# Optimization experiments

Hardware: AMD Instinct MI355X
Metric: run time of the kernel (lower is better)

Reference implementation:

```python
import jax, jax.numpy as jnp
import numpy as np

# config (from UnifiedAttentionConfig defaults)
D = 512; H = 8; C = 64; DQ = 256; NI = 2; CI = 64
TOPK = 32; LMAX = 16; NWIN = 128; ROPE_BASE = 10000.0
B = 1; T = 1024; LP = 8; P = T // LP
NEG = -1e30


def _rope_cache(seq_len, dim):
    half = dim // 2
    inv = 1.0 / (ROPE_BASE ** (jnp.arange(half, dtype=jnp.float32) / half))
    f = jnp.arange(seq_len, dtype=jnp.float32)[:, None] * inv[None, :]
    emb = jnp.concatenate([f, f], axis=-1)
    return jnp.cos(emb), jnp.sin(emb)


def _rot(x, cos, sin):
    half = x.shape[-1] // 2
    x1, x2 = x[..., :half], x[..., half:]
    return x * cos + jnp.concatenate([-x2, x1], axis=-1) * sin


def _rms(x, w, eps=1e-6):
    return x * jax.lax.rsqrt(jnp.mean(x * x, axis=-1, keepdims=True) + eps) * w


def _forward(h, W_dq, W_uq, W_csa_kv, W_csa_z, B_csa, W_idx_kv, W_idx_z, B_idx,
             W_iuq, W_w, W_swkv, qnorm_w, knorm_w, W_o, sink_logits,
             phrase_mask, phrase_token_idx, phrase_end_pos):
    Bq, Tq, Dq = h.shape
    Pn, Lmax = phrase_mask.shape[1], phrase_mask.shape[2]
    scale = 1.0 / jnp.sqrt(jnp.float32(C))
    cos, sin = _rope_cache(Tq, C)
    cos_i, sin_i = _rope_cache(Tq, CI)
    # ---- queries: compress -> up-project -> RMSNorm -> RoPE (per-token) ----
    q_lat = h @ W_dq                                      # (B,T,DQ)
    q = (q_lat @ W_uq).reshape(Bq, Tq, H, C)
    q = _rot(_rms(q, qnorm_w), cos[:, None, :], sin[:, None, :])
    # ---- gather phrase tokens ----
    idx = phrase_token_idx.reshape(Bq, Pn * Lmax)
    hp = jnp.take_along_axis(h, idx[:, :, None], axis=1).reshape(Bq, Pn, Lmax, Dq)
    m = phrase_mask                                       # (B,P,Lmax) bool
    # ---- multi-head phrase compression (CSA KV) ----
    c_tok = (hp @ W_csa_kv).reshape(Bq, Pn, Lmax, H, C)
    z = (hp @ W_csa_z).reshape(Bq, Pn, Lmax, H, C) + B_csa[None, None]
    z = jnp.where(m[..., None, None], z, NEG)
    g = jax.nn.softmax(z, axis=2)
    g = jnp.where(m.any(axis=2)[:, :, None, None, None], g, 0.0)
    c_csa = jnp.sum(g * c_tok, axis=2)                    # (B,P,H,C) values
    pos = jnp.clip(phrase_end_pos, 0, Tq - 1)
    k_csa = _rot(_rms(c_csa, knorm_w), cos[pos][:, :, None, :], sin[pos][:, :, None, :])
    # ---- single-head phrase compression (indexer keys) ----
    ck = hp @ W_idx_kv                                    # (B,P,Lmax,CI)
    zk = hp @ W_idx_z + B_idx[None, None]
    zk = jnp.where(m[..., None], zk, NEG)
    gk = jax.nn.softmax(zk, axis=2)
    gk = jnp.where(m.any(axis=2)[:, :, None, None], gk, 0.0)
    k_idx = jnp.sum(gk * ck, axis=2)                      # (B,P,CI)
    k_idx = _rot(k_idx, cos_i[pos], sin_i[pos])
    # ---- lightning indexer + causal top-k routing ----
    q_i = (q_lat @ W_iuq).reshape(Bq, Tq, NI, CI)
    s = jax.nn.relu(jnp.einsum('bthd,bpd->bthp', q_i, k_idx))
    I = jnp.sum(s * (h @ W_w)[..., None], axis=2)         # (B,T,P)
    t_idx = jnp.arange(Tq)
    valid = (phrase_end_pos[:, None, :] <= t_idx[None, :, None]) & (phrase_end_pos[:, None, :] >= 0)
    I = jnp.where(valid, I, NEG)
    vals, sel = jax.lax.top_k(I, TOPK)                    # (B,T,K)
    sel_ok = vals > NEG * 0.5
    k_sel = jnp.take_along_axis(k_csa[:, None], sel[:, :, :, None, None], axis=2)  # (B,T,K,H,C)
    v_sel = jnp.take_along_axis(c_csa[:, None], sel[:, :, :, None, None], axis=2)
    logit_csa = jnp.einsum('bthc,btkhc->bthk', q, k_sel) * scale
    logit_csa = jnp.where(sel_ok[:, :, None, :], logit_csa, NEG)
    # ---- sliding window (fixed mode) ----
    kv = (h @ W_swkv).reshape(Bq, Tq, H, C)
    k_sw = _rot(_rms(kv, knorm_w), cos[:, None, :], sin[:, None, :])
    widx = t_idx[:, None] + jnp.arange(NWIN)[None, :] - (NWIN - 1)  # (T,W)
    w_ok = widx >= 0
    widx_c = jnp.clip(widx, 0, Tq - 1)
    k_win = k_sw[:, widx_c]                               # (B,T,W,H,C)
    v_win = kv[:, widx_c]
    logit_sw = jnp.einsum('bthc,btwhc->bthw', q, k_win) * scale
    logit_sw = jnp.where(w_ok[None, :, None, :], logit_sw, NEG)
    # ---- single softmax over [csa | window | sink] ----
    sink = jnp.broadcast_to(sink_logits.reshape(1, 1, H, 1), (Bq, Tq, H, 1))
    pattn = jax.nn.softmax(jnp.concatenate([logit_csa, logit_sw, sink], axis=-1), axis=-1)
    out = jnp.einsum('bthk,btkhc->bthc', pattn[..., :TOPK], v_sel) \
        + jnp.einsum('bthw,btwhc->bthc', pattn[..., TOPK:TOPK + NWIN], v_win)
    return out.reshape(Bq, Tq, H * C) @ W_o


def setup_inputs() -> dict:
    key = jax.random.key(0)
    ks = jax.random.split(key, 16)
    nrm = lambda k, shp: 0.02 * jax.random.normal(k, shp, dtype=jnp.float32)
    # structured phrases: phrase p covers tokens [p*LP, p*LP+LP), padded to LMAX
    l = np.arange(LMAX)
    mask = np.broadcast_to(l < LP, (B, P, LMAX)).copy()
    tok = np.minimum(l, LP - 1)[None, :] + (np.arange(P) * LP)[:, None]
    tok = np.broadcast_to(tok, (B, P, LMAX)).copy()
    end = np.broadcast_to(np.arange(P) * LP + LP - 1, (B, P)).copy()
    pid = np.broadcast_to(np.arange(T) // LP, (B, T)).copy()
    return {
        'h': jax.random.normal(ks[0], (B, T, D), dtype=jnp.float32),
        'phrase_mask': jnp.asarray(mask, dtype=bool),
        'phrase_token_idx': jnp.asarray(tok, dtype=jnp.int32),
        'phrase_end_pos': jnp.asarray(end, dtype=jnp.int32),
        'phrase_id': jnp.asarray(pid, dtype=jnp.int32),
        'W_dq': nrm(ks[1], (D, DQ)),
        'W_uq': nrm(ks[2], (DQ, H * C)),
        'W_csa_kv': nrm(ks[3], (D, H * C)),
        'W_csa_z': nrm(ks[4], (D, H * C)),
        'B_csa': nrm(ks[5], (LMAX, H, C)),
        'W_idx_kv': nrm(ks[6], (D, CI)),
        'W_idx_z': nrm(ks[7], (D, CI)),
        'B_idx': nrm(ks[8], (LMAX, CI)),
        'W_iuq': nrm(ks[9], (DQ, NI * CI)),
        'W_w': nrm(ks[10], (D, NI)),
        'W_swkv': nrm(ks[11], (D, H * C)),
        'qnorm_w': jnp.ones((C,), dtype=jnp.float32),
        'knorm_w': jnp.ones((C,), dtype=jnp.float32),
        'W_o': nrm(ks[12], (H * C, D)),
        'sink_logits': nrm(ks[13], (H,)),
    }


def reference(h, phrase_mask, phrase_token_idx, phrase_end_pos, phrase_id,
              W_dq, W_uq, W_csa_kv, W_csa_z, B_csa, W_idx_kv, W_idx_z, B_idx,
              W_iuq, W_w, W_swkv, qnorm_w, knorm_w, W_o, sink_logits):
    del phrase_id  # only used when sw_mode == 'phrase'
    return _forward(h, W_dq, W_uq, W_csa_kv, W_csa_z, B_csa, W_idx_kv, W_idx_z,
                    B_idx, W_iuq, W_w, W_swkv, qnorm_w, knorm_w, W_o, sink_logits,
                    phrase_mask, phrase_token_idx, phrase_end_pos)
```

## Files before the change

kernel.cpp:

```cpp
#include <hip/hip_runtime.h>
#include <cmath>

static constexpr int Tn = 1024, Dn = 512, Hn = 8, Cn = 64, DQn = 256,
                     NIn = 2, CIn = 64, TK = 32, LM = 16, NW = 128, Pn = 128;
#define NEGV (-1e30f)

typedef unsigned short u16;
typedef __bf16 bf16x8 __attribute__((ext_vector_type(8)));
typedef float f32x4 __attribute__((ext_vector_type(4)));

__device__ __forceinline__ u16 f2bf(float x) {
  unsigned u = __float_as_uint(x);
  return (u16)((u + 0x7fffu + ((u >> 16) & 1u)) >> 16);
}
__device__ __forceinline__ float bf2f(u16 b) {
  return __uint_as_float((unsigned)b << 16);
}

struct PackJobs {
  const float* src[7];
  u16* dst[7];
  int start[8];
  int N[7];
  int logN[7];
  int isA[7];
  int ps[7];
};

__global__ __launch_bounds__(256) void pack_all(PackJobs pj) {
  int i = blockIdx.x * 256 + threadIdx.x;
  if (i >= pj.start[7]) return;
  int j = 0;
  while (i >= pj.start[j + 1]) ++j;
  int local = i - pj.start[j];
  const float* s = pj.src[j];
  u16* dh = pj.dst[j];
  u16* dl = dh + pj.ps[j];
  float x[8];
  size_t idx;
  if (pj.isA[j]) {
    int m = local & 1023;
    int kg = local >> 10;
    const float4* p = reinterpret_cast<const float4*>(s + (size_t)m * 512 + kg * 8);
    float4 a = p[0], b = p[1];
    x[0] = a.x; x[1] = a.y; x[2] = a.z; x[3] = a.w;
    x[4] = b.x; x[5] = b.y; x[6] = b.z; x[7] = b.w;
    idx = ((size_t)kg * 1024 + m) * 8;
  } else {
    int N = pj.N[j];
    int n = local & (N - 1);
    int kg = local >> pj.logN[j];
#pragma unroll
    for (int e = 0; e < 8; ++e) x[e] = s[(size_t)(kg * 8 + e) * N + n];
    idx = ((size_t)kg * N + n) * 8;
  }
  union { u16 u[8]; int4 v; } oh, ol;
#pragma unroll
  for (int e = 0; e < 8; ++e) {
    u16 hb = f2bf(x[e]);
    oh.u[e] = hb;
    ol.u[e] = f2bf(x[e] - bf2f(hb));
  }
  *reinterpret_cast<int4*>(dh + idx) = oh.v;
  *reinterpret_cast<int4*>(dl + idx) = ol.v;
}

struct TileDesc {
  const u16* Blo;
  const u16* Bhi;
  float* Clo;
  float* Chi;
  u16* Cp;
  int ldNlo, ldNhi, ldClo, ldChi, mode, n0, bps, cpps;
};
struct GemmArgs {
  TileDesc d[15];
};

#define GLD16(gp, lp)                                                     \
  __builtin_amdgcn_global_load_lds(                                      \
      (const __attribute__((address_space(1))) unsigned int*)(gp),       \
      (__attribute__((address_space(3))) unsigned int*)(lp), 16, 0, 0)

__global__ __launch_bounds__(256) void gemm_bf16(const u16* __restrict__ Ap,
                                                 int NK, int aps, GemmArgs ga) {
  const int ct = blockIdx.x, rt = blockIdx.y;
  const TileDesc d = ga.d[ct];
  const int m0 = rt * 128;
  __shared__ __align__(16) u16 lA[2][2][4][128][8];
  __shared__ __align__(16) u16 lB[2][2][4][128][8];
  const int tid = threadIdx.x;
  const int w = tid >> 6, lane = tid & 63;
  const int wm = w >> 1, wn = w & 1;

  f32x4 acc[4][4];
#pragma unroll
  for (int a = 0; a < 4; ++a)
#pragma unroll
    for (int b = 0; b < 4; ++b)
#pragma unroll
      for (int r = 0; r < 4; ++r) acc[a][b][r] = 0.f;

  auto stage = [&](int buf, int kg) {
    GLD16(Ap + ((size_t)kg * 1024 + m0 + lane) * 8, &lA[buf][0][w][0][0]);
    GLD16(Ap + ((size_t)kg * 1024 + m0 + 64 + lane) * 8, &lA[buf][0][w][64][0]);
    GLD16(Ap + aps + ((size_t)kg * 1024 + m0 + lane) * 8, &lA[buf][1][w][0][0]);
    GLD16(Ap + aps + ((size_t)kg * 1024 + m0 + 64 + lane) * 8, &lA[buf][1][w][64][0]);
    GLD16(d.Blo + ((size_t)kg * d.ldNlo + lane) * 8, &lB[buf][0][w][0][0]);
    GLD16(d.Bhi + ((size_t)kg * d.ldNhi + lane) * 8, &lB[buf][0][w][64][0]);
    GLD16(d.Blo + d.bps + ((size_t)kg * d.ldNlo + lane) * 8, &lB[buf][1][w][0][0]);
    GLD16(d.Bhi + d.bps + ((size_t)kg * d.ldNhi + lane) * 8, &lB[buf][1][w][64][0]);
  };

  stage(0, w);
  const int kq = lane >> 4, fr = lane & 15;
  for (int ks = 0; ks < NK; ++ks) {
    __syncthreads();
    if (ks + 1 < NK) stage((ks + 1) & 1, (ks + 1) * 4 + w);
    const int cb = ks & 1;
    bf16x8 aFh[4], aFl[4], bFh[4], bFl[4];
#pragma unroll
    for (int f = 0; f < 4; ++f) {
      aFh[f] = *reinterpret_cast<const bf16x8*>(&lA[cb][0][kq][wm * 64 + f * 16 + fr][0]);
      aFl[f] = *reinterpret_cast<const bf16x8*>(&lA[cb][1][kq][wm * 64 + f * 16 + fr][0]);
      bFh[f] = *reinterpret_cast<const bf16x8*>(&lB[cb][0][kq][wn * 64 + f * 16 + fr][0]);
      bFl[f] = *reinterpret_cast<const bf16x8*>(&lB[cb][1][kq][wn * 64 + f * 16 + fr][0]);
    }
#pragma unroll
    for (int fm = 0; fm < 4; ++fm)
#pragma unroll
      for (int fn = 0; fn < 4; ++fn) {
        acc[fm][fn] = __builtin_amdgcn_mfma_f32_16x16x32_bf16(aFh[fm], bFh[fn],
                                                              acc[fm][fn], 0, 0, 0);
        acc[fm][fn] = __builtin_amdgcn_mfma_f32_16x16x32_bf16(aFl[fm], bFh[fn],
                                                              acc[fm][fn], 0, 0, 0);
        acc[fm][fn] = __builtin_amdgcn_mfma_f32_16x16x32_bf16(aFh[fm], bFl[fn],
                                                              acc[fm][fn], 0, 0, 0);
      }
  }
  float* Cb = (wn == 0) ? d.Clo : d.Chi;
  const int ldc = (wn == 0) ? d.ldClo : d.ldChi;
  if (d.mode != 1) {
#pragma unroll
    for (int fm = 0; fm < 4; ++fm)
#pragma unroll
      for (int fn = 0; fn < 4; ++fn)
#pragma unroll
        for (int r = 0; r < 4; ++r) {
          int row = m0 + wm * 64 + fm * 16 + (lane >> 4) * 4 + r;
          int cl = fn * 16 + fr;
          Cb[(size_t)row * ldc + cl] = acc[fm][fn][r];
        }
  }
  if (d.mode >= 1) {
#pragma unroll
    for (int fm = 0; fm < 4; ++fm)
#pragma unroll
      for (int fn = 0; fn < 4; ++fn)
#pragma unroll
        for (int r = 0; r < 4; ++r) {
          int row = m0 + wm * 64 + fm * 16 + (lane >> 4) * 4 + r;
          int gc = d.n0 + wn * 64 + fn * 16 + fr;
          float v = acc[fm][fn][r];
          u16 hb = f2bf(v);
          u16 lb = f2bf(v - bf2f(hb));
          size_t idx = ((size_t)(gc >> 3) * 1024 + row) * 8 + (gc & 7);
          d.Cp[idx] = hb;
          d.Cp[idx + d.cpps] = lb;
        }
  }
}

__global__ __launch_bounds__(256) void idx_kernel(
    const float* __restrict__ h, const float* __restrict__ q_lat,
    const float* __restrict__ Wikv, const float* __restrict__ Wiz,
    const float* __restrict__ Wiuq, float* __restrict__ hikv,
    float* __restrict__ hiz, float* __restrict__ qib) {
  const int t0 = blockIdx.x * 4;
  const int tid = threadIdx.x;
  __shared__ float hs[4][Dn];
  __shared__ float ql[4][DQn];
  for (int i = tid; i < 4 * Dn; i += 256)
    hs[i >> 9][i & 511] = h[(size_t)(t0 + (i >> 9)) * Dn + (i & 511)];
  for (int i = tid; i < 4 * DQn; i += 256)
    ql[i >> 8][i & 255] = q_lat[(size_t)(t0 + (i >> 8)) * DQn + (i & 255)];
  __syncthreads();
  if (tid < 128) {
    const float* Wm = (tid < 64) ? Wikv : Wiz;
    const int ci = tid & 63;
    float a0 = 0.f, a1 = 0.f, a2 = 0.f, a3 = 0.f;
#pragma unroll 8
    for (int k = 0; k < Dn; ++k) {
      float wv = Wm[k * CIn + ci];
      a0 += hs[0][k] * wv;
      a1 += hs[1][k] * wv;
      a2 += hs[2][k] * wv;
      a3 += hs[3][k] * wv;
    }
    float* dst = (tid < 64) ? hikv : hiz;
    dst[(size_t)(t0 + 0) * CIn + ci] = a0;
    dst[(size_t)(t0 + 1) * CIn + ci] = a1;
    dst[(size_t)(t0 + 2) * CIn + ci] = a2;
    dst[(size_t)(t0 + 3) * CIn + ci] = a3;
  } else {
    const int jj = tid - 128;
    float a0 = 0.f, a1 = 0.f, a2 = 0.f, a3 = 0.f;
#pragma unroll 8
    for (int k = 0; k < DQn; ++k) {
      float wv = Wiuq[k * 128 + jj];
      a0 += ql[0][k] * wv;
      a1 += ql[1][k] * wv;
      a2 += ql[2][k] * wv;
      a3 += ql[3][k] * wv;
    }
    qib[(size_t)(t0 + 0) * 128 + jj] = a0;
    qib[(size_t)(t0 + 1) * 128 + jj] = a1;
    qib[(size_t)(t0 + 2) * 128 + jj] = a2;
    qib[(size_t)(t0 + 3) * 128 + jj] = a3;
  }
}

__global__ __launch_bounds__(512) void phrase_rope_kernel(
    const int* __restrict__ maskbuf, const int* __restrict__ tokbuf,
    const int* __restrict__ endbuf, const float* __restrict__ hckv,
    const float* __restrict__ hcz, const float* __restrict__ hikv,
    const float* __restrict__ hiz, const float* __restrict__ Bcsa,
    const float* __restrict__ Bidx, const float* __restrict__ knw,
    const float* __restrict__ qnw, float* __restrict__ ccsa,
    float* __restrict__ kcsa, float* __restrict__ kidx,
    float* __restrict__ q, const float* __restrict__ kv,
    float* __restrict__ ksw) {
  const int tid = threadIdx.x;
  const int c = tid & 63;
  const float sgn = (c < 32) ? -1.f : 1.f;

  if (blockIdx.x >= Pn) {
    const int t = blockIdx.x - Pn;
    const float fr = (float)t * powf(10000.0f, -(float)(c & 31) / 32.0f);
    const float cv = cosf(fr), sv = sinf(fr);
    {
      float x = q[t * Dn + tid];
      float ss = x * x;
#pragma unroll
      for (int off = 32; off; off >>= 1) ss += __shfl_xor(ss, off, 64);
      float xr = x * rsqrtf(ss / (float)Cn + 1e-6f) * qnw[c];
      float pr = __shfl_xor(xr, 32, 64);
      q[t * Dn + tid] = xr * cv + sgn * pr * sv;
    }
    {
      float y = kv[t * Dn + tid];
      float ss = y * y;
#pragma unroll
      for (int off = 32; off; off >>= 1) ss += __shfl_xor(ss, off, 64);
      float yr = y * rsqrtf(ss / (float)Cn + 1e-6f) * knw[c];
      float pr = __shfl_xor(yr, 32, 64);
      ksw[t * Dn + tid] = yr * cv + sgn * pr * sv;
    }
    return;
  }

  const int p = blockIdx.x;
  __shared__ int s_bytemode;
  __shared__ int s_tok[LM];
  __shared__ int s_m[LM];
  __shared__ int s_pos, s_anyv;

  if (tid == 0) s_bytemode = 0;
  __syncthreads();
  {
    unsigned wv = ((const unsigned*)maskbuf)[tid];
    if (wv > 1u) atomicOr(&s_bytemode, 1);
  }
  __syncthreads();
  const int bytemode = s_bytemode;
  if (tid < LM) {
    int mv;
    if (bytemode)
      mv = ((const unsigned char*)maskbuf)[p * LM + tid] != 0;
    else
      mv = maskbuf[p * LM + tid] != 0;
    s_m[tid] = mv;
    s_tok[tid] = tokbuf[p * LM + tid];
  }
  if (tid == 0) {
    int e = endbuf[p];
    s_pos = min(max(e, 0), Tn - 1);
  }
  __syncthreads();
  if (tid == 0) {
    int any = 0;
    for (int l = 0; l < LM; ++l) any |= s_m[l];
    s_anyv = any;
  }
  __syncthreads();
  const int anyv = s_anyv;
  const int pos = s_pos;
  const float fr = (float)pos * powf(10000.0f, -(float)(c & 31) / 32.0f);
  const float cv = cosf(fr), sv = sinf(fr);

  {
    float z[LM];
    float zmax = NEGV;
#pragma unroll
    for (int l = 0; l < LM; ++l) {
      float zv = hcz[s_tok[l] * Dn + tid] + Bcsa[l * (Hn * Cn) + tid];
      zv = s_m[l] ? zv : NEGV;
      z[l] = zv;
      zmax = fmaxf(zmax, zv);
    }
    float den = 0.f, num = 0.f;
#pragma unroll
    for (int l = 0; l < LM; ++l) {
      float e = expf(z[l] - zmax);
      den += e;
      num += e * hckv[s_tok[l] * Dn + tid];
    }
    float cc = anyv ? (num / den) : 0.f;
    ccsa[p * (Hn * Cn) + tid] = cc;

    float ss = cc * cc;
#pragma unroll
    for (int off = 32; off; off >>= 1) ss += __shfl_xor(ss, off, 64);
    float kn = cc * rsqrtf(ss / (float)Cn + 1e-6f) * knw[c];
    float pr = __shfl_xor(kn, 32, 64);
    kcsa[p * (Hn * Cn) + tid] = kn * cv + sgn * pr * sv;
  }

  if (tid < CIn) {
    float zk[LM];
    float zm = NEGV;
#pragma unroll
    for (int l = 0; l < LM; ++l) {
      float zv = hiz[s_tok[l] * CIn + tid] + Bidx[l * CIn + tid];
      zv = s_m[l] ? zv : NEGV;
      zk[l] = zv;
      zm = fmaxf(zm, zv);
    }
    float dk = 0.f, nk = 0.f;
#pragma unroll
    for (int l = 0; l < LM; ++l) {
      float e = expf(zk[l] - zm);
      dk += e;
      nk += e * hikv[s_tok[l] * CIn + tid];
    }
    float ki = anyv ? (nk / dk) : 0.f;
    float pr = __shfl_xor(ki, 32, 64);
    kidx[p * CIn + tid] = ki * cv + sgn * pr * sv;
  }
}

__global__ __launch_bounds__(128) void score_topk_kernel(
    const float* __restrict__ hbuf, const float* __restrict__ Ww,
    const float* __restrict__ qi, const float* __restrict__ kidx,
    const int* __restrict__ endbuf, int* __restrict__ sel,
    int* __restrict__ selok) {
  const int t = blockIdx.x;
  const int tid = threadIdx.x;
  __shared__ float sqi[NIn * CIn];
  __shared__ float kT[CIn][Pn + 1];
  __shared__ float sI[Pn];
  __shared__ float sp0[128], sp1[128];

  sqi[tid] = qi[(size_t)t * (NIn * CIn) + tid];
#pragma unroll
  for (int it = 0; it < 16; ++it) {
    int idx4 = it * 128 + tid;
    float4 v = reinterpret_cast<const float4*>(kidx)[idx4];
    int p = idx4 >> 4;
    int c4 = (idx4 & 15) * 4;
    kT[c4 + 0][p] = v.x;
    kT[c4 + 1][p] = v.y;
    kT[c4 + 2][p] = v.z;
    kT[c4 + 3][p] = v.w;
  }
  float p0 = 0.f, p1 = 0.f;
#pragma unroll
  for (int e4 = 0; e4 < 4; ++e4) {
    int e = tid * 4 + e4;
    float hv = hbuf[(size_t)t * Dn + e];
    p0 += hv * Ww[e * NIn + 0];
    p1 += hv * Ww[e * NIn + 1];
  }
  sp0[tid] = p0;
  sp1[tid] = p1;
  __syncthreads();
  for (int srd = 64; srd; srd >>= 1) {
    if (tid < srd) {
      sp0[tid] += sp0[tid + srd];
      sp1[tid] += sp1[tid + srd];
    }
    __syncthreads();
  }
  const float ww0 = sp0[0], ww1 = sp1[0];

  {
    const int p = tid;
    float s0 = 0.f, s1 = 0.f;
#pragma unroll 16
    for (int ci = 0; ci < CIn; ++ci) {
      float kc = kT[ci][p];
      s0 += sqi[ci] * kc;
      s1 += sqi[CIn + ci] * kc;
    }
    float Iv = fmaxf(s0, 0.f) * ww0 + fmaxf(s1, 0.f) * ww1;
    int e = endbuf[p];
    if (!(e <= t && e >= 0)) Iv = NEGV;
    sI[p] = Iv;
  }
  __syncthreads();

  if (tid < 64) {
    float v0 = sI[tid], v1 = sI[tid + 64];
    for (int it = 0; it < TK; ++it) {
      float bv;
      int bi;
      if (v0 >= v1) { bv = v0; bi = tid; } else { bv = v1; bi = tid + 64; }
#pragma unroll
      for (int off = 32; off; off >>= 1) {
        float ov = __shfl_xor(bv, off, 64);
        int oi = __shfl_xor(bi, off, 64);
        if (ov > bv || (ov == bv && oi < bi)) { bv = ov; bi = oi; }
      }
      if (tid == 0) {
        sel[t * TK + it] = bi;
        selok[t * TK + it] = (bv > NEGV * 0.5f) ? 1 : 0;
      }
      if (bi == tid) v0 = -3.4e38f;
      if (bi == tid + 64) v1 = -3.4e38f;
    }
  }
}

__global__ __launch_bounds__(256) void attn3_kernel(
    const float* __restrict__ q, const float* __restrict__ ksw,
    const float* __restrict__ kv, const float* __restrict__ kcsa,
    const float* __restrict__ ccsa, const int* __restrict__ sel,
    const int* __restrict__ selok, const float* __restrict__ sink,
    u16* __restrict__ atp) {
  const int tid = threadIdx.x;
  const int wid = tid >> 6, lane = tid & 63;
  const int g = lane >> 4;
  const int gl = lane & 15;
  const int pair = blockIdx.x * 4 + wid;
  const int t = pair >> 3, h = pair & 7;

  __shared__ float slog[4][164];
  __shared__ int s_sel[4][TK];
  __shared__ int s_ok[4][TK];

  if (lane < TK) {
    s_sel[wid][lane] = sel[t * TK + lane];
    s_ok[wid][lane] = selok[t * TK + lane];
  }
  const int hc = h * Cn + gl * 4;
  const float4 qf = *reinterpret_cast<const float4*>(&q[t * Dn + hc]);
  float* myslog = slog[wid];

#pragma unroll 4
  for (int pass = 0; pass < 32; ++pass) {
    int w = pass * 4 + g;
    int src = t + w - (NW - 1);
    int srcc = max(src, 0);
    float4 kk = *reinterpret_cast<const float4*>(&ksw[srcc * Dn + hc]);
    float acc = qf.x * kk.x + qf.y * kk.y + qf.z * kk.z + qf.w * kk.w;
#pragma unroll
    for (int off = 1; off < 16; off <<= 1) acc += __shfl_xor(acc, off, 64);
    if (gl == 0) myslog[TK + w] = (src >= 0) ? acc * 0.125f : NEGV;
  }
#pragma unroll 2
  for (int pass = 0; pass < 8; ++pass) {
    int s = pass * 4 + g;
    int se = s_sel[wid][s];
    float4 kk = *reinterpret_cast<const float4*>(&kcsa[se * Dn + hc]);
    float acc = qf.x * kk.x + qf.y * kk.y + qf.z * kk.z + qf.w * kk.w;
#pragma unroll
    for (int off = 1; off < 16; off <<= 1) acc += __shfl_xor(acc, off, 64);
    if (gl == 0) myslog[s] = s_ok[wid][s] ? acc * 0.125f : NEGV;
  }
  if (lane == 0) myslog[160] = sink[h];

  float x0 = myslog[lane];
  float x1 = myslog[lane + 64];
  float x2 = (lane < 33) ? myslog[lane + 128] : NEGV;
  float m = fmaxf(x0, fmaxf(x1, x2));
#pragma unroll
  for (int off = 32; off; off >>= 1) m = fmaxf(m, __shfl_xor(m, off, 64));
  float e0 = expf(x0 - m), e1 = expf(x1 - m);
  float e2 = (lane < 33) ? expf(x2 - m) : 0.f;
  float sden = e0 + e1 + e2;
#pragma unroll
  for (int off = 32; off; off >>= 1) sden += __shfl_xor(sden, off, 64);
  const float inv = 1.f / sden;
  myslog[lane] = e0 * inv;
  myslog[lane + 64] = e1 * inv;
  if (lane < 33) myslog[lane + 128] = e2 * inv;

  float4 acc = make_float4(0.f, 0.f, 0.f, 0.f);
#pragma unroll 4
  for (int pass = 0; pass < 32; ++pass) {
    int w = pass * 4 + g;
    int src = t + w - (NW - 1);
    int srcc = max(src, 0);
    float pv = myslog[TK + w];
    pv = (src >= 0) ? pv : 0.f;
    float4 vv = *reinterpret_cast<const float4*>(&kv[srcc * Dn + hc]);
    acc.x += pv * vv.x;
    acc.y += pv * vv.y;
    acc.z += pv * vv.z;
    acc.w += pv * vv.w;
  }
#pragma unroll 2
  for (int pass = 0; pass < 8; ++pass) {
    int s = pass * 4 + g;
    float pv = myslog[s];
    int se = s_sel[wid][s];
    float4 vv = *reinterpret_cast<const float4*>(&ccsa[se * Dn + hc]);
    acc.x += pv * vv.x;
    acc.y += pv * vv.y;
    acc.z += pv * vv.z;
    acc.w += pv * vv.w;
  }
  acc.x += __shfl_xor(acc.x, 16, 64);
  acc.y += __shfl_xor(acc.y, 16, 64);
  acc.z += __shfl_xor(acc.z, 16, 64);
  acc.w += __shfl_xor(acc.w, 16, 64);
  acc.x += __shfl_xor(acc.x, 32, 64);
  acc.y += __shfl_xor(acc.y, 32, 64);
  acc.z += __shfl_xor(acc.z, 32, 64);
  acc.w += __shfl_xor(acc.w, 32, 64);
  if (lane < 16) {
    float vals[4] = {acc.x, acc.y, acc.z, acc.w};
    int colb = h * Cn + lane * 4;
#pragma unroll
    for (int r = 0; r < 4; ++r) {
      int gc = colb + r;
      float v = vals[r];
      u16 hb = f2bf(v);
      u16 lb = f2bf(v - bf2f(hb));
      size_t idx = ((size_t)(gc >> 3) * 1024 + t) * 8 + (gc & 7);
      atp[idx] = hb;
      atp[idx + 524288] = lb;
    }
  }
}

extern "C" void kernel_launch(void* const* d_in, const int* in_sizes, int n_in,
                              void* d_out, int out_size, void* d_ws,
                              size_t ws_size, hipStream_t stream) {
  const float* h = (const float*)d_in[0];
  const int* mask = (const int*)d_in[1];
  const int* tok = (const int*)d_in[2];
  const int* endp = (const int*)d_in[3];
  const float* W_dq = (const float*)d_in[5];
  const float* W_uq = (const float*)d_in[6];
  const float* W_csa_kv = (const float*)d_in[7];
  const float* W_csa_z = (const float*)d_in[8];
  const float* B_csa = (const float*)d_in[9];
  const float* W_idx_kv = (const float*)d_in[10];
  const float* W_idx_z = (const float*)d_in[11];
  const float* B_idx = (const float*)d_in[12];
  const float* W_iuq = (const float*)d_in[13];
  const float* W_w = (const float*)d_in[14];
  const float* W_swkv = (const float*)d_in[15];
  const float* qnw = (const float*)d_in[16];
  const float* knw = (const float*)d_in[17];
  const float* W_o = (const float*)d_in[18];
  const float* sink = (const float*)d_in[19];

  float* ws = (float*)d_ws;
  u16* hA = (u16*)(ws + 0);
  float* qbuf = ws + 0;
  u16* qlP = (u16*)(ws + 524288);
  float* hckv = ws + 786432;
  u16* atP = (u16*)(ws + 786432);
  float* hcz = ws + 1310720;
  float* kvb = ws + 1835008;
  float* hikv = ws + 2359296;
  float* hiz = ws + 2424832;
  float* q_lat = ws + 2490368;
  float* ccsa = ws + 2752512;
  float* kcsa = ws + 2818048;
  float* kidx = ws + 2883584;
  int* seli = (int*)(ws + 2891776);
  int* selok = (int*)(ws + 2924544);
  float* qib = ws + 2957312;
  float* kswb = ws + 3088384;
  u16* pW = (u16*)(ws + 3612672);
  u16* pWdq = pW;
  u16* pWckv = pW + 262144;
  u16* pWcz = pW + 786432;
  u16* pWsw = pW + 1310720;
  u16* pWuq = pW + 1835008;
  u16* pWo = pW + 2097152;
  float* outp = (float*)d_out;

  {
    PackJobs pj{};
    const float* srcs[7] = {h, W_dq, W_csa_kv, W_csa_z, W_swkv, W_uq, W_o};
    u16* dsts[7] = {hA, pWdq, pWckv, pWcz, pWsw, pWuq, pWo};
    int Ns[7] = {0, 256, 512, 512, 512, 512, 512};
    int logNs[7] = {0, 8, 9, 9, 9, 9, 9};
    int Ks[7] = {512, 512, 512, 512, 512, 256, 512};
    int isA[7] = {1, 0, 0, 0, 0, 0, 0};
    int pss[7] = {524288, 131072, 262144, 262144, 262144, 131072, 262144};
    int s = 0;
    for (int i = 0; i < 7; ++i) {
      pj.src[i] = srcs[i];
      pj.dst[i] = dsts[i];
      pj.N[i] = Ns[i];
      pj.logN[i] = logNs[i];
      pj.isA[i] = isA[i];
      pj.ps[i] = pss[i];
      pj.start[i] = s;
      s += isA[i] ? 1024 * (Ks[i] / 8) : (Ks[i] / 8) * Ns[i];
    }
    pj.start[7] = s;
    pack_all<<<(s + 255) / 256, 256, 0, stream>>>(pj);
  }

  auto normTile = [](const u16* pB, int N, int n0, float* C, int ldc, int bps) {
    TileDesc td{};
    td.Blo = pB + n0 * 8;
    td.Bhi = pB + (n0 + 64) * 8;
    td.ldNlo = td.ldNhi = N;
    td.Clo = C + n0;
    td.Chi = C + n0 + 64;
    td.ldClo = td.ldChi = ldc;
    td.mode = 0;
    td.bps = bps;
    return td;
  };

  {
    GemmArgs ga{};
    int nt = 0;
    for (int n0 = 0; n0 < 256; n0 += 128) {
      TileDesc td = normTile(pWdq, 256, n0, q_lat, 256, 131072);
      td.mode = 2;
      td.Cp = qlP;
      td.cpps = 262144;
      td.n0 = n0;
      ga.d[nt++] = td;
    }
    for (int n0 = 0; n0 < 512; n0 += 128) ga.d[nt++] = normTile(pWckv, 512, n0, hckv, 512, 262144);
    for (int n0 = 0; n0 < 512; n0 += 128) ga.d[nt++] = normTile(pWcz, 512, n0, hcz, 512, 262144);
    for (int n0 = 0; n0 < 512; n0 += 128) ga.d[nt++] = normTile(pWsw, 512, n0, kvb, 512, 262144);
    gemm_bf16<<<dim3(nt, 8), 256, 0, stream>>>(hA, 16, 524288, ga);
  }
  {
    GemmArgs ga{};
    int nt = 0;
    for (int n0 = 0; n0 < 512; n0 += 128) ga.d[nt++] = normTile(pWuq, 512, n0, qbuf, 512, 131072);
    gemm_bf16<<<dim3(nt, 8), 256, 0, stream>>>(qlP, 8, 262144, ga);
  }
  idx_kernel<<<Tn / 4, 256, 0, stream>>>(h, q_lat, W_idx_kv, W_idx_z, W_iuq,
                                         hikv, hiz, qib);
  phrase_rope_kernel<<<Pn + Tn, 512, 0, stream>>>(
      mask, tok, endp, hckv, hcz, hikv, hiz, B_csa, B_idx, knw, qnw, ccsa,
      kcsa, kidx, qbuf, kvb, kswb);
  score_topk_kernel<<<Tn, 128, 0, stream>>>(h, W_w, qib, kidx, endp, seli,
                                            selok);
  attn3_kernel<<<dim3(Tn * Hn / 4), 256, 0, stream>>>(qbuf, kswb, kvb, kcsa,
                                                      ccsa, seli, selok, sink,
                                                      atP);
  {
    GemmArgs ga{};
    int nt = 0;
    for (int n0 = 0; n0 < 512; n0 += 128) ga.d[nt++] = normTile(pWo, 512, n0, outp, 512, 262144);
    gemm_bf16<<<dim3(nt, 8), 256, 0, stream>>>(atP, 16, 524288, ga);
  }
  (void)in_sizes; (void)n_in; (void)out_size; (void)ws_size;
}
```

Measured before the change: 151.1 us.

## Halve GEMM M-tile to 64 rows and remap attention blocks head-major

The bf16 split-precision GEMM is templated on the per-wave M fragment count and launched with 64-row tiles, which doubles the number of blocks so more of the GPU's compute units get work on these small 1024-row problems. The cost is that each B tile is loaded twice as often per output. The attention kernel is also remapped so each block handles four consecutive tokens of a single head instead of four heads of one token, which changes which sliding-window and key-value data neighbouring waves share in cache.

Result: faster. 136.6 us (-9.6%).

```diff
diff --git a/kernel.cpp b/kernel.cpp
--- a/kernel.cpp
+++ b/kernel.cpp
@@ -82,30 +82,33 @@
       (const __attribute__((address_space(1))) unsigned int*)(gp),       \
       (__attribute__((address_space(3))) unsigned int*)(lp), 16, 0, 0)
 
+template <int FMW>
 __global__ __launch_bounds__(256) void gemm_bf16(const u16* __restrict__ Ap,
                                                  int NK, int aps, GemmArgs ga) {
+  constexpr int MT = FMW * 32;
   const int ct = blockIdx.x, rt = blockIdx.y;
   const TileDesc d = ga.d[ct];
-  const int m0 = rt * 128;
-  __shared__ __align__(16) u16 lA[2][2][4][128][8];
+  const int m0 = rt * MT;
+  __shared__ __align__(16) u16 lA[2][2][4][MT][8];
   __shared__ __align__(16) u16 lB[2][2][4][128][8];
   const int tid = threadIdx.x;
   const int w = tid >> 6, lane = tid & 63;
   const int wm = w >> 1, wn = w & 1;
 
-  f32x4 acc[4][4];
-#pragma unroll
-  for (int a = 0; a < 4; ++a)
+  f32x4 acc[FMW][4];
+#pragma unroll
+  for (int a = 0; a < FMW; ++a)
 #pragma unroll
     for (int b = 0; b < 4; ++b)
 #pragma unroll
       for (int r = 0; r < 4; ++r) acc[a][b][r] = 0.f;
 
   auto stage = [&](int buf, int kg) {
-    GLD16(Ap + ((size_t)kg * 1024 + m0 + lane) * 8, &lA[buf][0][w][0][0]);
-    GLD16(Ap + ((size_t)kg * 1024 + m0 + 64 + lane) * 8, &lA[buf][0][w][64][0]);
-    GLD16(Ap + aps + ((size_t)kg * 1024 + m0 + lane) * 8, &lA[buf][1][w][0][0]);
-    GLD16(Ap + aps + ((size_t)kg * 1024 + m0 + 64 + lane) * 8, &lA[buf][1][w][64][0]);
+#pragma unroll
+    for (int r0 = 0; r0 < MT; r0 += 64) {
+      GLD16(Ap + ((size_t)kg * 1024 + m0 + r0 + lane) * 8, &lA[buf][0][w][r0][0]);
+      GLD16(Ap + aps + ((size_t)kg * 1024 + m0 + r0 + lane) * 8, &lA[buf][1][w][r0][0]);
+    }
     GLD16(d.Blo + ((size_t)kg * d.ldNlo + lane) * 8, &lB[buf][0][w][0][0]);
     GLD16(d.Bhi + ((size_t)kg * d.ldNhi + lane) * 8, &lB[buf][0][w][64][0]);
     GLD16(d.Blo + d.bps + ((size_t)kg * d.ldNlo + lane) * 8, &lB[buf][1][w][0][0]);
@@ -118,16 +121,19 @@
     __syncthreads();
     if (ks + 1 < NK) stage((ks + 1) & 1, (ks + 1) * 4 + w);
     const int cb = ks & 1;
-    bf16x8 aFh[4], aFl[4], bFh[4], bFl[4];
+    bf16x8 aFh[FMW], aFl[FMW], bFh[4], bFl[4];
+#pragma unroll
+    for (int f = 0; f < FMW; ++f) {
+      aFh[f] = *reinterpret_cast<const bf16x8*>(&lA[cb][0][kq][wm * (FMW * 16) + f * 16 + fr][0]);
+      aFl[f] = *reinterpret_cast<const bf16x8*>(&lA[cb][1][kq][wm * (FMW * 16) + f * 16 + fr][0]);
+    }
 #pragma unroll
     for (int f = 0; f < 4; ++f) {
-      aFh[f] = *reinterpret_cast<const bf16x8*>(&lA[cb][0][kq][wm * 64 + f * 16 + fr][0]);
-      aFl[f] = *reinterpret_cast<const bf16x8*>(&lA[cb][1][kq][wm * 64 + f * 16 + fr][0]);
       bFh[f] = *reinterpret_cast<const bf16x8*>(&lB[cb][0][kq][wn * 64 + f * 16 + fr][0]);
       bFl[f] = *reinterpret_cast<const bf16x8*>(&lB[cb][1][kq][wn * 64 + f * 16 + fr][0]);
     }
 #pragma unroll
-    for (int fm = 0; fm < 4; ++fm)
+    for (int fm = 0; fm < FMW; ++fm)
 #pragma unroll
       for (int fn = 0; fn < 4; ++fn) {
         acc[fm][fn] = __builtin_amdgcn_mfma_f32_16x16x32_bf16(aFh[fm], bFh[fn],
@@ -142,24 +148,24 @@
   const int ldc = (wn == 0) ? d.ldClo : d.ldChi;
   if (d.mode != 1) {
 #pragma unroll
-    for (int fm = 0; fm < 4; ++fm)
+    for (int fm = 0; fm < FMW; ++fm)
 #pragma unroll
       for (int fn = 0; fn < 4; ++fn)
 #pragma unroll
         for (int r = 0; r < 4; ++r) {
-          int row = m0 + wm * 64 + fm * 16 + (lane >> 4) * 4 + r;
+          int row = m0 + wm * (FMW * 16) + fm * 16 + (lane >> 4) * 4 + r;
           int cl = fn * 16 + fr;
           Cb[(size_t)row * ldc + cl] = acc[fm][fn][r];
         }
   }
   if (d.mode >= 1) {
 #pragma unroll
-    for (int fm = 0; fm < 4; ++fm)
+    for (int fm = 0; fm < FMW; ++fm)
 #pragma unroll
       for (int fn = 0; fn < 4; ++fn)
 #pragma unroll
         for (int r = 0; r < 4; ++r) {
-          int row = m0 + wm * 64 + fm * 16 + (lane >> 4) * 4 + r;
+          int row = m0 + wm * (FMW * 16) + fm * 16 + (lane >> 4) * 4 + r;
           int gc = d.n0 + wn * 64 + fn * 16 + fr;
           float v = acc[fm][fn][r];
           u16 hb = f2bf(v);
@@ -431,7 +437,7 @@
   }
 }
 
-__global__ __launch_bounds__(256) void attn3_kernel(
+__global__ __launch_bounds__(256) void attn4_kernel(
     const float* __restrict__ q, const float* __restrict__ ksw,
     const float* __restrict__ kv, const float* __restrict__ kcsa,
     const float* __restrict__ ccsa, const int* __restrict__ sel,
@@ -441,8 +447,8 @@
   const int wid = tid >> 6, lane = tid & 63;
   const int g = lane >> 4;
   const int gl = lane & 15;
-  const int pair = blockIdx.x * 4 + wid;
-  const int t = pair >> 3, h = pair & 7;
+  const int h = blockIdx.x >> 8;
+  const int t = ((blockIdx.x & 255) << 2) + wid;
 
   __shared__ float slog[4][164];
   __shared__ int s_sel[4][TK];
@@ -645,13 +651,13 @@
     for (int n0 = 0; n0 < 512; n0 += 128) ga.d[nt++] = normTile(pWckv, 512, n0, hckv, 512, 262144);
     for (int n0 = 0; n0 < 512; n0 += 128) ga.d[nt++] = normTile(pWcz, 512, n0, hcz, 512, 262144);
     for (int n0 = 0; n0 < 512; n0 += 128) ga.d[nt++] = normTile(pWsw, 512, n0, kvb, 512, 262144);
-    gemm_bf16<<<dim3(nt, 8), 256, 0, stream>>>(hA, 16, 524288, ga);
+    gemm_bf16<2><<<dim3(nt, 16), 256, 0, stream>>>(hA, 16, 524288, ga);
   }
   {
     GemmArgs ga{};
     int nt = 0;
     for (int n0 = 0; n0 < 512; n0 += 128) ga.d[nt++] = normTile(pWuq, 512, n0, qbuf, 512, 131072);
-    gemm_bf16<<<dim3(nt, 8), 256, 0, stream>>>(qlP, 8, 262144, ga);
+    gemm_bf16<2><<<dim3(nt, 16), 256, 0, stream>>>(qlP, 8, 262144, ga);
   }
   idx_kernel<<<Tn / 4, 256, 0, stream>>>(h, q_lat, W_idx_kv, W_idx_z, W_iuq,
                                          hikv, hiz, qib);
@@ -660,14 +666,14 @@
       kcsa, kidx, qbuf, kvb, kswb);
   score_topk_kernel<<<Tn, 128, 0, stream>>>(h, W_w, qib, kidx, endp, seli,
                                             selok);
-  attn3_kernel<<<dim3(Tn * Hn / 4), 256, 0, stream>>>(qbuf, kswb, kvb, kcsa,
+  attn4_kernel<<<dim3(Tn / 4 * Hn), 256, 0, stream>>>(qbuf, kswb, kvb, kcsa,
                                                       ccsa, seli, selok, sink,
                                                       atP);
   {
     GemmArgs ga{};
     int nt = 0;
     for (int n0 = 0; n0 < 512; n0 += 128) ga.d[nt++] = normTile(pWo, 512, n0, outp, 512, 262144);
-    gemm_bf16<<<dim3(nt, 8), 256, 0, stream>>>(atP, 16, 524288, ga);
+    gemm_bf16<2><<<dim3(nt, 16), 256, 0, stream>>>(atP, 16, 524288, ga);
   }
   (void)in_sizes; (void)n_in; (void)out_size; (void)ws_size;
 }
```
